# Kernel tuning notes

Measured on AMD Instinct MI355X. Metric: run time of the kernel, lower is better.

The kernel has to match this reference:

```python
import jax, jax.numpy as jnp
import numpy as np

B, T, D, H, HD = 2, 2048, 1024, 16, 64
EPS = 1.1920929e-07  # torch.finfo(float32).eps used by F.rms_norm default
VE_GATE_SCALE = 2.0
KEY_OFFSET = True


def rms_norm(x):
    return x * jax.lax.rsqrt(jnp.mean(x * x, axis=-1, keepdims=True) + EPS)


def apply_rotary(x, cos, sin):
    # x: [B,T,H,HD], cos/sin: [T, HD//2]
    c = cos[None, :, None, :]
    s = sin[None, :, None, :]
    x1, x2 = jnp.split(x, 2, axis=-1)
    return jnp.concatenate([x1 * c + x2 * s, -x1 * s + x2 * c], axis=-1)


def setup_inputs() -> dict:
    key = jax.random.key(0)
    ks = jax.random.split(key, 8)
    bound = (3.0 ** 0.5) * (D ** -0.5)
    x = jax.random.normal(ks[0], (B, T, D), dtype=jnp.float32)
    ve = jax.random.normal(ks[1], (B, T, H * HD), dtype=jnp.float32)
    sa_lambdas = jnp.ones((2,), dtype=jnp.float32)
    # realistic RoPE tables
    inv_freq = (10000.0 ** (-np.arange(HD // 2) / (HD // 2))).astype(np.float32)
    ang = np.arange(T, dtype=np.float32)[:, None] * inv_freq[None, :]
    cos = jnp.asarray(np.cos(ang))
    sin = jnp.asarray(np.sin(ang))
    # qkvo weight: uniform init everywhere (orig zeros o-proj; randomized for a non-trivial baseline)
    qkvo_w = jax.random.uniform(ks[2], (4 * D, D), dtype=jnp.float32, minval=-bound, maxval=bound)
    attn_gate_w = 0.02 * jax.random.normal(ks[3], (H, D), dtype=jnp.float32)
    ve_gate_w = 0.02 * jax.random.normal(ks[4], (H, D), dtype=jnp.float32)
    attn_scale = jnp.float32(0.12)
    docs = jnp.sort(jax.random.randint(ks[5], (T,), 0, 8).astype(jnp.int32))
    return {"x": x, "ve": ve, "sa_lambdas": sa_lambdas, "cos": cos, "sin": sin,
            "qkvo_w": qkvo_w, "attn_gate_w": attn_gate_w, "ve_gate_w": ve_gate_w,
            "attn_scale": attn_scale, "docs": docs}


def reference(x, ve, sa_lambdas, cos, sin, qkvo_w, attn_gate_w, ve_gate_w, attn_scale, docs):
    # QKV projection: rows [0:3D] of qkvo_w
    qkv = jnp.einsum('btd,ed->bte', x, sa_lambdas[0] * qkvo_w[:3 * D])
    qkv = qkv.reshape(B, T, 3 * H, HD)
    q, k, v = qkv[:, :, :H], qkv[:, :, H:2 * H], qkv[:, :, 2 * H:]
    q, k = rms_norm(q), rms_norm(k)
    q, k = apply_rotary(q, cos, sin), apply_rotary(k, cos, sin)
    if KEY_OFFSET:
        # shift two head-dim bands of k forward by one position
        k = k.at[:, 1:, :, HD // 4:HD // 2].set(k[:, :-1, :, HD // 4:HD // 2])
        k = k.at[:, 1:, :, 3 * HD // 4:].set(k[:, :-1, :, 3 * HD // 4:])
    # gated value embedding
    ve_gate = VE_GATE_SCALE * jax.nn.sigmoid(jnp.einsum('btd,hd->bth', x, ve_gate_w))
    v = v + ve_gate[..., None] * ve.reshape(B, T, H, HD)
    # causal + document masked attention (score_mod semantics)
    idx = jnp.arange(T)
    mask = (idx[:, None] >= idx[None, :]) & (docs[:, None] == docs[None, :])  # [T,T]
    scores = jnp.einsum('bqhd,bkhd->bhqk', q, k) * attn_scale
    scores = jnp.where(mask[None, None], scores, -jnp.inf)
    p = jax.nn.softmax(scores, axis=-1)
    y = jnp.einsum('bhqk,bkhd->bqhd', p, v)
    # attention output gate
    attn_gate = jax.nn.sigmoid(jnp.einsum('btd,hd->bth', x, attn_gate_w))
    y = y * attn_gate[..., None]
    # output projection: rows [3D:4D]
    y = y.reshape(B, T, H * HD)
    out = jnp.einsum('btd,ed->bte', y, sa_lambdas[1] * qkvo_w[3 * D:])
    return out
```

## Files before the change

kernel.cpp:

```cpp
#include <hip/hip_runtime.h>
#include <math.h>

#define B_ 2
#define T_ 2048
#define D_ 1024
#define H_ 16
#define HD_ 64
#define EPS_ 1.1920929e-07f
#define VE_SCALE_ 2.0f

#define NX4_ (B_ * T_ * D_ / 4)
#define NS4_ (3 * D_ * D_ / 4)
#define NQ4_ (4 * D_ * D_ / 4)
#define NG4_ (H_ * D_ / 4)

typedef __bf16 bf16_t;
typedef __bf16 bf16x4 __attribute__((ext_vector_type(4)));
typedef __bf16 bf16x8 __attribute__((ext_vector_type(8)));
typedef float f32x4 __attribute__((ext_vector_type(4)));

__device__ const f32x4 F4ZERO = {0.f, 0.f, 0.f, 0.f};

typedef __attribute__((address_space(1))) const void gvoid_t;
typedef __attribute__((address_space(3))) void lvoid_t;

__device__ __forceinline__ void gl_lds16(const bf16_t* g, bf16_t* l) {
  __builtin_amdgcn_global_load_lds((gvoid_t*)g, (lvoid_t*)l, 16, 0, 0);
}

__global__ __launch_bounds__(256) void cast_all(
    const float* __restrict__ x, const float* __restrict__ qkvo,
    const float* __restrict__ agw, const float* __restrict__ vgw,
    bf16_t* __restrict__ x_bf, bf16_t* __restrict__ wq,
    bf16_t* __restrict__ wo, bf16_t* __restrict__ wg)
{
  const int i = blockIdx.x * 256 + threadIdx.x;
  const float4* src;
  bf16x4* dst;
  if (i < NX4_) {
    src = (const float4*)x + i;
    dst = (bf16x4*)x_bf + i;
  } else if (i < NX4_ + NS4_) {
    const int j = i - NX4_;
    src = (const float4*)qkvo + j;
    dst = (bf16x4*)wq + j;
  } else if (i < NX4_ + NQ4_) {
    const int j = i - NX4_;
    src = (const float4*)qkvo + j;
    dst = (bf16x4*)wo + (j - NS4_);
  } else if (i < NX4_ + NQ4_ + NG4_) {
    const int j = i - NX4_ - NQ4_;
    src = (const float4*)agw + j;
    dst = (bf16x4*)wg + j;
  } else {
    const int j = i - NX4_ - NQ4_ - NG4_;
    src = (const float4*)vgw + j;
    dst = (bf16x4*)wg + NG4_ + j;
  }
  const float4 v = *src;
  bf16x4 o = {(bf16_t)v.x, (bf16_t)v.y, (bf16_t)v.z, (bf16_t)v.w};
  *dst = o;
}

__global__ __launch_bounds__(256) void gemm_bf16(
    const bf16_t* __restrict__ A, const bf16_t* __restrict__ W,
    void* __restrict__ Cout, int M, int N, int K,
    const float* __restrict__ lam, int li, int out_bf)
{
  const float scale = lam[li];
  __shared__ bf16_t As[128][32];
  __shared__ bf16_t Bs[128][32];
  const int tid = threadIdx.x;
  const int lane = tid & 63, w = tid >> 6;
  const int lr = lane & 15, lg = lane >> 4;
  const int wr = w >> 1, wc = w & 1;

  const int nwg = gridDim.x * gridDim.y;
  int bid = blockIdx.y * gridDim.x + blockIdx.x;
  bid = (bid & 7) * (nwg >> 3) + (bid >> 3);
  const int row0 = (bid / gridDim.x) * 128;
  const int col0 = (bid % gridDim.x) * 128;

  const int srow = w * 32 + (lane >> 2);
  const int scol = (lane & 3) * 8;
  const bf16_t* Ag = A + (size_t)(row0 + srow) * K + scol;
  const bf16_t* Wg = W + (size_t)(col0 + srow) * K + scol;
  bf16_t* AsB0 = &As[w * 32][0];
  bf16_t* AsB1 = &As[w * 32 + 16][0];
  bf16_t* BsB0 = &Bs[w * 32][0];
  bf16_t* BsB1 = &Bs[w * 32 + 16][0];
  const size_t r16 = (size_t)16 * K;

  f32x4 acc[4][4];
#pragma unroll
  for (int i = 0; i < 4; ++i)
#pragma unroll
    for (int j = 0; j < 4; ++j) acc[i][j] = F4ZERO;

  for (int k0 = 0; k0 < K; k0 += 32) {
    __syncthreads();
    gl_lds16(Ag + k0, AsB0);
    gl_lds16(Ag + r16 + k0, AsB1);
    gl_lds16(Wg + k0, BsB0);
    gl_lds16(Wg + r16 + k0, BsB1);
    __syncthreads();

    bf16x8 af[4], bfr[4];
#pragma unroll
    for (int fm = 0; fm < 4; ++fm)
      af[fm] = *(const bf16x8*)&As[wr * 64 + fm * 16 + lr][lg * 8];
#pragma unroll
    for (int fn = 0; fn < 4; ++fn)
      bfr[fn] = *(const bf16x8*)&Bs[wc * 64 + fn * 16 + lr][lg * 8];
#pragma unroll
    for (int fm = 0; fm < 4; ++fm)
#pragma unroll
      for (int fn = 0; fn < 4; ++fn)
        acc[fm][fn] = __builtin_amdgcn_mfma_f32_16x16x32_bf16(
            af[fm], bfr[fn], acc[fm][fn], 0, 0, 0);
  }
#pragma unroll
  for (int fm = 0; fm < 4; ++fm)
#pragma unroll
    for (int fn = 0; fn < 4; ++fn)
#pragma unroll
      for (int r = 0; r < 4; ++r) {
        const int row = row0 + wr * 64 + fm * 16 + lg * 4 + r;
        const int col = col0 + wc * 64 + fn * 16 + lr;
        const float v = acc[fm][fn][r] * scale;
        if (out_bf) ((bf16_t*)Cout)[(size_t)row * N + col] = (bf16_t)v;
        else        ((float*)Cout)[(size_t)row * N + col] = v;
      }
}

__global__ __launch_bounds__(256) void post_kernel(
    const float* __restrict__ x, const bf16_t* __restrict__ qkv_b,
    const float* __restrict__ ve, const float* __restrict__ cosb,
    const float* __restrict__ sinb, const bf16_t* __restrict__ wg,
    bf16_t* __restrict__ q_bf, bf16_t* __restrict__ k_bf,
    bf16_t* __restrict__ v_bf, float* __restrict__ attn_gate)
{
  const int bt = blockIdx.x;
  const int b = bt >> 11, t = bt & (T_ - 1);
  const int tid = threadIdx.x;
  __shared__ float xs[D_];
  __shared__ float gsc[32];

  *(float4*)&xs[tid * 4] = ((const float4*)(x + (size_t)bt * D_))[tid];
  __syncthreads();

  {
    const int g = tid >> 3, cg = tid & 7;
    const bf16x8* wrow = (const bf16x8*)(wg + (size_t)g * D_);
    float sum = 0.f;
#pragma unroll
    for (int j = 0; j < 16; ++j) {
      const bf16x8 w8 = wrow[cg + 8 * j];
      const float* xp = &xs[(cg + 8 * j) * 8];
#pragma unroll
      for (int e = 0; e < 8; ++e) sum = fmaf((float)w8[e], xp[e], sum);
    }
    sum += __shfl_xor(sum, 1);
    sum += __shfl_xor(sum, 2);
    sum += __shfl_xor(sum, 4);
    if (cg == 0)
      gsc[g] = (g < 16 ? 1.f : VE_SCALE_) / (1.f + __expf(-sum));
  }
  __syncthreads();

  const int w = tid >> 6, lane = tid & 63;
  const float c = cosb[t * 32 + (lane & 31)];
  const float s = sinb[t * 32 + (lane & 31)];
  const size_t row = (size_t)bt * 3072;
#pragma unroll
  for (int i = 0; i < 4; ++i) {
    const int h = w + i * 4;
    const float qraw = (float)qkv_b[row + h * HD_ + lane];
    const float kraw = (float)qkv_b[row + D_ + h * HD_ + lane];
    const float vraw = (float)qkv_b[row + 2 * D_ + h * HD_ + lane];
    float ssq = qraw * qraw, ssk = kraw * kraw;
#pragma unroll
    for (int off = 32; off > 0; off >>= 1) {
      ssq += __shfl_xor(ssq, off);
      ssk += __shfl_xor(ssk, off);
    }
    const float qn = qraw * rsqrtf(ssq * (1.f / 64.f) + EPS_);
    const float kn = kraw * rsqrtf(ssk * (1.f / 64.f) + EPS_);
    const float qpartner = __shfl_xor(qn, 32);
    const float kpartner = __shfl_xor(kn, 32);
    const float qo = (lane < 32) ? fmaf(qn, c, qpartner * s)
                                 : fmaf(qn, c, -qpartner * s);
    const float ko = (lane < 32) ? fmaf(kn, c, kpartner * s)
                                 : fmaf(kn, c, -kpartner * s);
    const size_t oidx = ((size_t)(b * H_ + h) * T_ + t) * HD_ + lane;
    q_bf[oidx] = (bf16_t)qo;
    k_bf[oidx] = (bf16_t)ko;
    const float vv = fmaf(gsc[16 + h], ve[(size_t)bt * D_ + h * HD_ + lane], vraw);
    v_bf[oidx] = (bf16_t)vv;
    if (lane == 0) attn_gate[bt * H_ + h] = gsc[h];
  }
}

__global__ __launch_bounds__(256) void attn_mfma(
    const bf16_t* __restrict__ q_buf, const bf16_t* __restrict__ k_tmp,
    const bf16_t* __restrict__ v_buf, const float* __restrict__ attn_gate,
    const int* __restrict__ docs, const float* __restrict__ scale_ptr,
    bf16_t* __restrict__ y_buf)
{
  const int qt = blockIdx.x, bh = blockIdx.y;
  const int b = bh >> 4, h = bh & 15;
  const int tid = threadIdx.x;
  const int w = tid >> 6, lane = tid & 63;
  const int lr = lane & 15, lg = lane >> 4;
  const float scale = scale_ptr[0];
  __shared__ bf16_t Ks[64][72];
  __shared__ bf16_t Vt[64][72];
  __shared__ bf16_t Ps[64][72];
  __shared__ int dk[64];

  const int dlo = docs[qt * 64];
  const unsigned long long bal =
      __ballot((lane <= qt) && (docs[lane * 64 + 63] >= dlo));
  const int ktlo = __ffsll(bal) - 1;

  const bf16_t* qp = q_buf + ((size_t)bh * T_ + qt * 64 + w * 16 + lr) * HD_;
  const bf16x8 aq0 = *(const bf16x8*)(qp + lg * 8);
  const bf16x8 aq1 = *(const bf16x8*)(qp + 32 + lg * 8);
  int qpos_r[4], docq_r[4];
#pragma unroll
  for (int r = 0; r < 4; ++r) {
    qpos_r[r] = qt * 64 + w * 16 + lg * 4 + r;
    docq_r[r] = docs[qpos_r[r]];
  }
  f32x4 acc[4];
#pragma unroll
  for (int fn = 0; fn < 4; ++fn) acc[fn] = F4ZERO;
  float m[4] = {-1e30f, -1e30f, -1e30f, -1e30f};
  float l[4] = {0.f, 0.f, 0.f, 0.f};

#pragma unroll 1
  for (int kt = ktlo; kt <= qt; ++kt) {
    __syncthreads();
#pragma unroll
    for (int i = 0; i < 2; ++i) {
      const int idx = i * 256 + tid;
      const int krow = idx >> 3;
      const int c8 = (idx & 7) << 3;
      const int gk = kt * 64 + krow;
      const int gks = (((c8 & 16) != 0) && gk > 0) ? gk - 1 : gk;
      *(bf16x8*)&Ks[krow][c8] =
          *(const bf16x8*)(k_tmp + ((size_t)bh * T_ + gks) * HD_ + c8);
      const int kpos = idx & 63;
      const int d0 = (idx >> 6) << 3;
      const bf16x8 vv =
          *(const bf16x8*)(v_buf + ((size_t)bh * T_ + kt * 64 + kpos) * HD_ + d0);
#pragma unroll
      for (int j = 0; j < 8; ++j) Vt[d0 + j][kpos] = vv[j];
    }
    if (tid < 64) dk[tid] = docs[kt * 64 + tid];
    __syncthreads();

    f32x4 s[4];
#pragma unroll
    for (int fn = 0; fn < 4; ++fn) {
      const bf16x8 bk0 = *(const bf16x8*)&Ks[fn * 16 + lr][lg * 8];
      const bf16x8 bk1 = *(const bf16x8*)&Ks[fn * 16 + lr][32 + lg * 8];
      f32x4 z = F4ZERO;
      z = __builtin_amdgcn_mfma_f32_16x16x32_bf16(aq0, bk0, z, 0, 0, 0);
      s[fn] = __builtin_amdgcn_mfma_f32_16x16x32_bf16(aq1, bk1, z, 0, 0, 0);
    }
    const bool strict = (kt < qt);
#pragma unroll
    for (int fn = 0; fn < 4; ++fn) {
      const int kd = dk[fn * 16 + lr];
      const int kp = kt * 64 + fn * 16 + lr;
#pragma unroll
      for (int r = 0; r < 4; ++r) {
        const bool valid = (kd == docq_r[r]) && (strict || kp <= qpos_r[r]);
        s[fn][r] = valid ? s[fn][r] * scale : -3.0e38f;
      }
    }
#pragma unroll
    for (int r = 0; r < 4; ++r) {
      float cm = fmaxf(fmaxf(s[0][r], s[1][r]), fmaxf(s[2][r], s[3][r]));
      cm = fmaxf(cm, __shfl_xor(cm, 1));
      cm = fmaxf(cm, __shfl_xor(cm, 2));
      cm = fmaxf(cm, __shfl_xor(cm, 4));
      cm = fmaxf(cm, __shfl_xor(cm, 8));
      const float mn = fmaxf(m[r], cm);
      const float sc = __expf(m[r] - mn);
      m[r] = mn;
      const float p0 = __expf(s[0][r] - mn);
      const float p1 = __expf(s[1][r] - mn);
      const float p2 = __expf(s[2][r] - mn);
      const float p3 = __expf(s[3][r] - mn);
      float ps = (p0 + p1) + (p2 + p3);
      ps += __shfl_xor(ps, 1);
      ps += __shfl_xor(ps, 2);
      ps += __shfl_xor(ps, 4);
      ps += __shfl_xor(ps, 8);
      l[r] = l[r] * sc + ps;
      acc[0][r] *= sc; acc[1][r] *= sc; acc[2][r] *= sc; acc[3][r] *= sc;
      const int prow = w * 16 + lg * 4 + r;
      Ps[prow][0 + lr]  = (bf16_t)p0;
      Ps[prow][16 + lr] = (bf16_t)p1;
      Ps[prow][32 + lr] = (bf16_t)p2;
      Ps[prow][48 + lr] = (bf16_t)p3;
    }
    const bf16x8 ap0 = *(const bf16x8*)&Ps[w * 16 + lr][lg * 8];
    const bf16x8 ap1 = *(const bf16x8*)&Ps[w * 16 + lr][32 + lg * 8];
#pragma unroll
    for (int fn = 0; fn < 4; ++fn) {
      const bf16x8 bv0 = *(const bf16x8*)&Vt[fn * 16 + lr][lg * 8];
      const bf16x8 bv1 = *(const bf16x8*)&Vt[fn * 16 + lr][32 + lg * 8];
      acc[fn] = __builtin_amdgcn_mfma_f32_16x16x32_bf16(ap0, bv0, acc[fn], 0, 0, 0);
      acc[fn] = __builtin_amdgcn_mfma_f32_16x16x32_bf16(ap1, bv1, acc[fn], 0, 0, 0);
    }
  }
#pragma unroll
  for (int r = 0; r < 4; ++r) {
    const float inv = attn_gate[(size_t)(b * T_ + qpos_r[r]) * H_ + h] / l[r];
#pragma unroll
    for (int fn = 0; fn < 4; ++fn)
      y_buf[(size_t)(b * T_ + qpos_r[r]) * D_ + h * HD_ + fn * 16 + lr] =
          (bf16_t)(acc[fn][r] * inv);
  }
}

extern "C" void kernel_launch(void* const* d_in, const int* in_sizes, int n_in,
                              void* d_out, int out_size, void* d_ws, size_t ws_size,
                              hipStream_t stream) {
  const float* x    = (const float*)d_in[0];
  const float* ve   = (const float*)d_in[1];
  const float* lam  = (const float*)d_in[2];
  const float* cosb = (const float*)d_in[3];
  const float* sinb = (const float*)d_in[4];
  const float* qkvo = (const float*)d_in[5];
  const float* agw  = (const float*)d_in[6];
  const float* vgw  = (const float*)d_in[7];
  const float* ascl = (const float*)d_in[8];
  const int*   docs = (const int*)d_in[9];
  float* out = (float*)d_out;

  const size_t BT = (size_t)B_ * T_;
  float* cur = (float*)d_ws;
  bf16_t* x_bf = (bf16_t*)cur;        cur += BT * D_ / 2;
  bf16_t* wq_bf = (bf16_t*)cur;       cur += (size_t)3 * D_ * D_ / 2;
  bf16_t* wo_bf = (bf16_t*)cur;       cur += (size_t)D_ * D_ / 2;
  bf16_t* wg_bf = (bf16_t*)cur;       cur += (size_t)2 * H_ * D_ / 2;
  bf16_t* qkv_b = (bf16_t*)cur;       cur += BT * 3 * D_ / 2;
  bf16_t* q_bf = (bf16_t*)cur;        cur += BT * D_ / 2;
  bf16_t* k_bf = (bf16_t*)cur;        cur += BT * D_ / 2;
  bf16_t* v_bf = (bf16_t*)cur;        cur += BT * D_ / 2;
  bf16_t* y_bf = (bf16_t*)cur;        cur += BT * D_ / 2;
  float* attn_gate = cur;             cur += BT * H_;

  cast_all<<<(NX4_ + NQ4_ + 2 * NG4_) / 256, 256, 0, stream>>>(
      x, qkvo, agw, vgw, x_bf, wq_bf, wo_bf, wg_bf);

  gemm_bf16<<<dim3(3 * D_ / 128, BT / 128), 256, 0, stream>>>(
      x_bf, wq_bf, qkv_b, (int)BT, 3 * D_, D_, lam, 0, 1);

  post_kernel<<<(int)BT, 256, 0, stream>>>(
      x, qkv_b, ve, cosb, sinb, wg_bf, q_bf, k_bf, v_bf, attn_gate);

  attn_mfma<<<dim3(T_ / 64, B_ * H_), 256, 0, stream>>>(
      q_bf, k_bf, v_bf, attn_gate, docs, ascl, y_bf);

  gemm_bf16<<<dim3(D_ / 128, BT / 128), 256, 0, stream>>>(
      y_bf, wo_bf, out, (int)BT, D_, D_, lam, 1, 0);
}
```

Baseline: 134.7 us.

## Double-buffer LDS tiles in bf16 GEMM to overlap loads with MFMA

```diff
diff --git a/kernel.cpp b/kernel.cpp
--- a/kernel.cpp
+++ b/kernel.cpp
@@ -68,8 +68,8 @@
     const float* __restrict__ lam, int li, int out_bf)
 {
   const float scale = lam[li];
-  __shared__ bf16_t As[128][32];
-  __shared__ bf16_t Bs[128][32];
+  __shared__ bf16_t As[2][128][32];
+  __shared__ bf16_t Bs[2][128][32];
   const int tid = threadIdx.x;
   const int lane = tid & 63, w = tid >> 6;
   const int lr = lane & 15, lg = lane >> 4;
@@ -85,10 +85,6 @@
   const int scol = (lane & 3) * 8;
   const bf16_t* Ag = A + (size_t)(row0 + srow) * K + scol;
   const bf16_t* Wg = W + (size_t)(col0 + srow) * K + scol;
-  bf16_t* AsB0 = &As[w * 32][0];
-  bf16_t* AsB1 = &As[w * 32 + 16][0];
-  bf16_t* BsB0 = &Bs[w * 32][0];
-  bf16_t* BsB1 = &Bs[w * 32 + 16][0];
   const size_t r16 = (size_t)16 * K;
 
   f32x4 acc[4][4];
@@ -97,28 +93,44 @@
 #pragma unroll
     for (int j = 0; j < 4; ++j) acc[i][j] = F4ZERO;
 
-  for (int k0 = 0; k0 < K; k0 += 32) {
+#define STAGE_(bi, kk)                                    \
+  do {                                                    \
+    gl_lds16(Ag + (kk), &As[bi][w * 32][0]);              \
+    gl_lds16(Ag + r16 + (kk), &As[bi][w * 32 + 16][0]);   \
+    gl_lds16(Wg + (kk), &Bs[bi][w * 32][0]);              \
+    gl_lds16(Wg + r16 + (kk), &Bs[bi][w * 32 + 16][0]);   \
+  } while (0)
+
+#define COMPUTE_(bi)                                                     \
+  do {                                                                   \
+    bf16x8 af[4], bfr[4];                                                \
+    _Pragma("unroll")                                                    \
+    for (int fm = 0; fm < 4; ++fm)                                       \
+      af[fm] = *(const bf16x8*)&As[bi][wr * 64 + fm * 16 + lr][lg * 8];  \
+    _Pragma("unroll")                                                    \
+    for (int fn = 0; fn < 4; ++fn)                                       \
+      bfr[fn] = *(const bf16x8*)&Bs[bi][wc * 64 + fn * 16 + lr][lg * 8]; \
+    _Pragma("unroll")                                                    \
+    for (int fm = 0; fm < 4; ++fm)                                       \
+      _Pragma("unroll")                                                  \
+      for (int fn = 0; fn < 4; ++fn)                                     \
+        acc[fm][fn] = __builtin_amdgcn_mfma_f32_16x16x32_bf16(           \
+            af[fm], bfr[fn], acc[fm][fn], 0, 0, 0);                      \
+  } while (0)
+
+  STAGE_(0, 0);
+  __syncthreads();
+  for (int k0 = 0; k0 + 64 <= K; k0 += 64) {
+    STAGE_(1, k0 + 32);
+    COMPUTE_(0);
     __syncthreads();
-    gl_lds16(Ag + k0, AsB0);
-    gl_lds16(Ag + r16 + k0, AsB1);
-    gl_lds16(Wg + k0, BsB0);
-    gl_lds16(Wg + r16 + k0, BsB1);
+    if (k0 + 64 < K) STAGE_(0, k0 + 64);
+    COMPUTE_(1);
     __syncthreads();
-
-    bf16x8 af[4], bfr[4];
-#pragma unroll
-    for (int fm = 0; fm < 4; ++fm)
-      af[fm] = *(const bf16x8*)&As[wr * 64 + fm * 16 + lr][lg * 8];
-#pragma unroll
-    for (int fn = 0; fn < 4; ++fn)
-      bfr[fn] = *(const bf16x8*)&Bs[wc * 64 + fn * 16 + lr][lg * 8];
-#pragma unroll
-    for (int fm = 0; fm < 4; ++fm)
-#pragma unroll
-      for (int fn = 0; fn < 4; ++fn)
-        acc[fm][fn] = __builtin_amdgcn_mfma_f32_16x16x32_bf16(
-            af[fm], bfr[fn], acc[fm][fn], 0, 0, 0);
-  }
+  }
+#undef STAGE_
+#undef COMPUTE_
+
 #pragma unroll
   for (int fm = 0; fm < 4; ++fm)
 #pragma unroll
```

Result: faster. 131.3 us (-2.5%).
